# Kernel tuning notes

Measured on AMD Instinct MI355X. Metric: run time of the kernel, lower is better.

## Reference

```python
import jax, jax.numpy as jnp
import numpy as np

# DeformConv (RegSeg): offset conv + mask conv (sigmoid) + modulated deformable conv v2
STRIDE = 1
PAD = 1
DIL = 1
G = 1          # deformable_groups
KH, KW = 3, 3


def _conv(x, w, b):
    # standard NCHW conv, stride/pad/dilation of the module
    y = jax.lax.conv_general_dilated(
        x, w, window_strides=(STRIDE, STRIDE),
        padding=((PAD, PAD), (PAD, PAD)), rhs_dilation=(DIL, DIL),
        dimension_numbers=("NCHW", "OIHW", "NCHW"))
    return y + b[None, :, None, None]


def _deform_conv2d(x, offset, mask, w, b):
    # torchvision DeformConv2d (modulated, v2) semantics
    B, C, H, W = x.shape
    O = w.shape[0]
    K = KH * KW
    Ho = (H + 2 * PAD - DIL * (KH - 1) - 1) // STRIDE + 1
    Wo = (W + 2 * PAD - DIL * (KW - 1) - 1) // STRIDE + 1
    Cg = C // G

    # base sampling grid: p0 + p_k
    ky = jnp.repeat(jnp.arange(KH), KW) * DIL            # [K]
    kx = jnp.tile(jnp.arange(KW), KH) * DIL              # [K]
    oy = jnp.arange(Ho) * STRIDE - PAD                   # [Ho]
    ox = jnp.arange(Wo) * STRIDE - PAD                   # [Wo]
    base_y = (ky[:, None, None] + oy[None, :, None]).astype(x.dtype)  # [K,Ho,1]
    base_x = (kx[:, None, None] + ox[None, None, :]).astype(x.dtype)  # [K,1,Wo]

    off = offset.reshape(B, G, K, 2, Ho, Wo)             # channel layout: g, k, (dy,dx)
    py = base_y[None, None] + off[:, :, :, 0]            # [B,G,K,Ho,Wo]
    px = base_x[None, None] + off[:, :, :, 1]
    m = mask.reshape(B, G, K, Ho, Wo)

    imgf = x.reshape(B * G, Cg, H * W)
    y0 = jnp.floor(py).astype(jnp.int32)
    x0 = jnp.floor(px).astype(jnp.int32)
    ly = py - y0.astype(x.dtype)
    lx = px - x0.astype(x.dtype)

    def corner(iy, ix, wgt):
        # zero-padded bilinear corner: out-of-bounds corners contribute 0
        valid = (iy >= 0) & (iy < H) & (ix >= 0) & (ix < W)
        idx = (jnp.clip(iy, 0, H - 1) * W + jnp.clip(ix, 0, W - 1)).reshape(B * G, -1)
        g = jax.vmap(lambda im, ii: im[:, ii])(imgf, idx)            # [B*G,Cg,K*Ho*Wo]
        g = g.reshape(B, G, Cg, K, Ho, Wo)
        return g * (wgt * valid.astype(x.dtype))[:, :, None]          # [B,G,Cg,K,Ho,Wo]

    val = (corner(y0,     x0,     (1 - ly) * (1 - lx))
         + corner(y0,     x0 + 1, (1 - ly) * lx)
         + corner(y0 + 1, x0,     ly * (1 - lx))
         + corner(y0 + 1, x0 + 1, ly * lx))
    val = val * m[:, :, None]                                         # modulation

    wr = w.reshape(O, G, Cg, K)
    out = jnp.einsum("bgckpq,ogck->bopq", val, wr) + b[None, :, None, None]
    return out


def setup_inputs() -> dict:
    key = jax.random.key(0)
    ks = jax.random.split(key, 8)
    B, C, H, W, O = 4, 128, 96, 96, 128
    K = KH * KW
    fan = 1.0 / np.sqrt(C * K)
    return {
        "x":        jax.random.normal(ks[0], (B, C, H, W), jnp.float32),
        "x2":       jax.random.normal(ks[1], (B, C, H, W), jnp.float32),
        "offset_w": jax.random.normal(ks[2], (2 * G * K, C, KH, KW), jnp.float32) * 0.01,
        "offset_b": jax.random.normal(ks[3], (2 * G * K,), jnp.float32) * 0.01,
        "mask_w":   jax.random.normal(ks[4], (G * K, C, KH, KW), jnp.float32) * 0.05,
        "mask_b":   jnp.zeros((G * K,), jnp.float32),
        "deform_w": jax.random.normal(ks[5], (O, C, KH, KW), jnp.float32) * fan,
        "deform_b": jax.random.normal(ks[6], (O,), jnp.float32) * fan,
    }


def reference(x, x2, offset_w, offset_b, mask_w, mask_b, deform_w, deform_b):
    offset = _conv(x2, offset_w, offset_b)
    mask = jax.nn.sigmoid(_conv(x2, mask_w, mask_b))
    return _deform_conv2d(x, offset, mask, deform_w, deform_b)
```

## Files before the change

kernel.cpp:

```cpp
#include <hip/hip_runtime.h>

#define CIN   128
#define HH    96
#define WW    96
#define OUTC  128
#define HWSZ  9216
#define KK    9
#define KTOT  1152

typedef _Float16 f16x8 __attribute__((ext_vector_type(8)));
typedef _Float16 h2    __attribute__((ext_vector_type(2)));
typedef float    f32x4 __attribute__((ext_vector_type(4)));

__device__ __forceinline__ unsigned short f2h(float f) {
  _Float16 h = (_Float16)f;
  return __builtin_bit_cast(unsigned short, h);
}
__device__ __forceinline__ unsigned pack_h(float v0, float v1) {
  auto r = __builtin_amdgcn_cvt_pkrtz(v0, v1);
  return __builtin_bit_cast(unsigned, r);
}

#define WT2B_O 147456
#define BIAS_O 184320
#define XN_O   184384
#define X2N_O  (184384 + 4718592)

__global__ __launch_bounds__(256) void prep_all(
    const float* __restrict__ x, const float* __restrict__ x2,
    const float* __restrict__ offw, const float* __restrict__ maskw,
    const float* __restrict__ defw, const float* __restrict__ offb,
    const float* __restrict__ maskb, void* __restrict__ wsv) {
  int bid = blockIdx.x;
  int t = threadIdx.x;
  if (bid < 1152) {
    __shared__ unsigned short tile[64][136];
    int tsel = bid / 576;
    int rem = bid - tsel * 576;
    int b = rem / 144;
    int hw0 = (rem % 144) * 64;
    const float* src = tsel ? x2 : x;
    unsigned short* dst = (unsigned short*)wsv + (tsel ? X2N_O : XN_O);
    unsigned* tw = (unsigned*)&tile[0][0];
    int c2  = t & 15;
    int px4 = t >> 4;
#pragma unroll
    for (int pass = 0; pass < 4; ++pass) {
      int c = pass * 32 + c2 * 2;
      const float* r0 = src + ((size_t)(b * CIN + c)) * HWSZ + hw0 + px4 * 4;
      float4 f0 = *(const float4*)r0;
      float4 f1 = *(const float4*)(r0 + HWSZ);
      int wb = pass * 16 + c2;
      tw[(px4 * 4 + 0) * 68 + wb] = pack_h(f0.x, f1.x);
      tw[(px4 * 4 + 1) * 68 + wb] = pack_h(f0.y, f1.y);
      tw[(px4 * 4 + 2) * 68 + wb] = pack_h(f0.z, f1.z);
      tw[(px4 * 4 + 3) * 68 + wb] = pack_h(f0.w, f1.w);
    }
    __syncthreads();
    unsigned* drow = (unsigned*)(dst + ((size_t)(b * HWSZ + hw0)) * 128);
    int w4 = t & 15, pxr = t >> 4;
#pragma unroll
    for (int pass = 0; pass < 4; ++pass) {
      int px = pass * 16 + pxr;
      uint4 v = *(const uint4*)&tw[px * 68 + w4 * 4];
      *(uint4*)&drow[(size_t)px * 64 + w4 * 4] = v;
    }
    return;
  }
  unsigned short* wtb  = (unsigned short*)wsv;
  unsigned short* wt2b = wtb + WT2B_O;
  float* bias32 = (float*)(wtb + BIAS_O);
  int idx = (bid - 1152) * 256 + t;
  if (idx < OUTC * KTOT) {
    int o = idx / KTOT, r = idx - o * KTOT;
    int c = r / KK, tap = r - c * KK;
    wtb[o * KTOT + tap * 128 + c] = f2h(defw[idx]);
  } else if (idx < OUTC * KTOT + 32 * KTOT) {
    int j = idx - OUTC * KTOT;
    int oc = j / KTOT, r = j - oc * KTOT;
    int c = r / KK, tap = r - c * KK;
    float v = 0.f;
    if (oc < 18)      v = offw[j];
    else if (oc < 27) v = maskw[j - 18 * KTOT];
    wt2b[oc * KTOT + tap * 128 + c] = f2h(v);
  } else if (idx < OUTC * KTOT + 32 * KTOT + 32) {
    int j = idx - OUTC * KTOT - 32 * KTOT;
    float v = 0.f;
    if (j < 18) v = offb[j]; else if (j < 27) v = maskb[j - 18];
    bias32[j] = v;
  }
}

__global__ __launch_bounds__(256, 2) void fused(
    const float* __restrict__ defb, const void* __restrict__ wsv,
    float* __restrict__ out) {
  const unsigned short* wtb  = (const unsigned short*)wsv;
  const unsigned short* wt2b = wtb + WT2B_O;
  const float* bias32 = (const float*)(wtb + BIAS_O);
  const unsigned short* xn  = wtb + XN_O;
  const unsigned short* x2n = wtb + X2N_O;

  __shared__ unsigned bwA[64 * 68];
  __shared__ unsigned bwB[64 * 68];
  __shared__ unsigned short val[64][136];
  __shared__ unsigned sidxw[KK * 4 * 64];
  float* om = (float*)&val[0][0];

  int t = threadIdx.x;
  int w = t >> 6;
  int mw = w & 1, nw = w >> 1;
  int l15 = t & 15, quad = (t >> 4) & 3;
  int rb = blockIdx.x;
  int bid = (rb & 7) * 72 + (rb >> 3);
  int b = bid / 144;
  int pblk = (bid % 144) * 64;

  int phg[4], pwg[4];
#pragma unroll
  for (int G = 0; G < 4; ++G) {
    int p = pblk + w * 16 + G * 4 + quad;
    phg[G] = p / WW;
    pwg[G] = p - phg[G] * WW;
  }

  f32x4 oa0 = {0.f, 0.f, 0.f, 0.f};
  f32x4 oa1 = {0.f, 0.f, 0.f, 0.f};
  const unsigned short* x2nb = x2n + ((size_t)b * HWSZ) * 128;
  for (int tap = 0; tap < KK; ++tap) {
    int ky = tap / 3 - 1, kx = tap % 3 - 1;
    uint4 vG[4];
#pragma unroll
    for (int G = 0; G < 4; ++G) {
      int y = phg[G] + ky, xx = pwg[G] + kx;
      bool ok = ((unsigned)y < HH) && ((unsigned)xx < WW);
      int pos = ok ? (y * WW + xx) : 0;
      uint4 v = *(const uint4*)(x2nb + ((size_t)pos << 7) + l15 * 8);
      vG[G] = ok ? v : make_uint4(0u, 0u, 0u, 0u);
    }
#pragma unroll
    for (int j = 0; j < 2; ++j) {
      int cc = t + 256 * j;
      int row = cc >> 4, c16 = cc & 15;
      *(uint4*)&bwA[row * 68 + c16 * 4] =
          *(const uint4*)(wt2b + (size_t)row * KTOT + tap * 128 + c16 * 8);
    }
#pragma unroll
    for (int G = 0; G < 4; ++G)
      *(uint4*)&val[w * 16 + G * 4 + quad][l15 * 8] = vG[G];
    __syncthreads();
#pragma unroll
    for (int ks = 0; ks < 4; ++ks) {
      f16x8 af = *(const f16x8*)&val[w * 16 + l15][ks * 32 + quad * 8];
      f16x8 b0 = *(const f16x8*)&bwA[(size_t)l15 * 68 + ks * 16 + quad * 4];
      f16x8 b1 = *(const f16x8*)&bwA[(size_t)(l15 + 16) * 68 + ks * 16 + quad * 4];
      oa0 = __builtin_amdgcn_mfma_f32_16x16x32_f16(af, b0, oa0, 0, 0, 0);
      oa1 = __builtin_amdgcn_mfma_f32_16x16x32_f16(af, b1, oa1, 0, 0, 0);
    }
    __syncthreads();
  }
#pragma unroll
  for (int nt = 0; nt < 2; ++nt) {
    f32x4 a = nt ? oa1 : oa0;
    int oc = nt * 16 + l15;
    float bia = bias32[oc];
#pragma unroll
    for (int r = 0; r < 4; ++r)
      om[oc * 68 + w * 16 + quad * 4 + r] = a[r] + bia;
  }
  __syncthreads();

  for (int e = t; e < KK * 64; e += 256) {
    int tap = e >> 6, pp = e & 63;
    int gp2 = pblk + pp;
    int h = gp2 / WW, ww_ = gp2 % WW;
    float dy = om[2 * tap * 68 + pp], dx = om[(2 * tap + 1) * 68 + pp];
    float mr = om[(18 + tap) * 68 + pp];
    float m = 1.f / (1.f + __expf(-mr));
    float py  = (float)(h + tap / 3 - 1) + dy;
    float pxx = (float)(ww_ + tap % 3 - 1) + dx;
    float y0f = floorf(py), x0f = floorf(pxx);
    int y0 = (int)y0f, x0 = (int)x0f;
    float ly = py - y0f, lx = pxx - x0f;
    int y1 = y0 + 1, x1 = x0 + 1;
    bool vy0 = (unsigned)y0 < HH, vy1 = (unsigned)y1 < HH;
    bool vx0 = (unsigned)x0 < WW, vx1 = (unsigned)x1 < WW;
    int cy0 = min(max(y0, 0), HH - 1), cy1 = min(max(y1, 0), HH - 1);
    int cx0 = min(max(x0, 0), WW - 1), cx1 = min(max(x1, 0), WW - 1);
    unsigned i00 = cy0 * WW + cx0, i01 = cy0 * WW + cx1;
    unsigned i10 = cy1 * WW + cx0, i11 = cy1 * WW + cx1;
    float w00 = (vy0 && vx0) ? m * (1.f - ly) * (1.f - lx) : 0.f;
    float w01 = (vy0 && vx1) ? m * (1.f - ly) * lx         : 0.f;
    float w10 = (vy1 && vx0) ? m * ly * (1.f - lx)         : 0.f;
    float w11 = (vy1 && vx1) ? m * ly * lx                 : 0.f;
    sidxw[(tap * 4 + 0) * 64 + pp] = i00 | ((unsigned)f2h(w00) << 16);
    sidxw[(tap * 4 + 1) * 64 + pp] = i01 | ((unsigned)f2h(w01) << 16);
    sidxw[(tap * 4 + 2) * 64 + pp] = i10 | ((unsigned)f2h(w10) << 16);
    sidxw[(tap * 4 + 3) * 64 + pp] = i11 | ((unsigned)f2h(w11) << 16);
  }
  __syncthreads();

  f32x4 acc[8];
#pragma unroll
  for (int nt = 0; nt < 8; ++nt) acc[nt] = (f32x4){0.f, 0.f, 0.f, 0.f};
  const unsigned short* xnb = xn + ((size_t)b * HWSZ) * 128;

  auto gatherT = [&](int tap, unsigned sw[4][4], uint4 v[4][4]) {
#pragma unroll
    for (int cr = 0; cr < 4; ++cr)
#pragma unroll
      for (int G = 0; G < 4; ++G)
        sw[cr][G] = sidxw[(tap * 4 + cr) * 64 + w * 16 + G * 4 + quad];
#pragma unroll
    for (int G = 0; G < 4; ++G)
#pragma unroll
      for (int cr = 0; cr < 4; ++cr)
        v[cr][G] = *(const uint4*)(xnb + ((size_t)(sw[cr][G] & 0xffffu) << 7) + l15 * 8);
  };
  auto combineT = [&](unsigned sw[4][4], uint4 v[4][4]) {
#pragma unroll
    for (int G = 0; G < 4; ++G) {
      h2 f[4];
#pragma unroll
      for (int j = 0; j < 4; ++j) f[j] = (h2){(_Float16)0.f, (_Float16)0.f};
#pragma unroll
      for (int cr = 0; cr < 4; ++cr) {
        _Float16 wh =
            __builtin_bit_cast(_Float16, (unsigned short)(sw[cr][G] >> 16));
        h2 wpk = {wh, wh};
        const h2* a = (const h2*)&v[cr][G];
#pragma unroll
        for (int j = 0; j < 4; ++j)
          f[j] += wpk * a[j];
      }
      *(uint4*)&val[w * 16 + G * 4 + quad][l15 * 8] =
          make_uint4(__builtin_bit_cast(unsigned, f[0]),
                     __builtin_bit_cast(unsigned, f[1]),
                     __builtin_bit_cast(unsigned, f[2]),
                     __builtin_bit_cast(unsigned, f[3]));
    }
  };
  auto stageHalf = [&](unsigned* buf, int tap, int half) {
#pragma unroll
    for (int j = 0; j < 4; ++j) {
      int cc = t + 256 * j;
      int row = cc >> 4, c16 = cc & 15;
      *(uint4*)&buf[row * 68 + c16 * 4] =
          *(const uint4*)(wtb + (size_t)(half * 64 + row) * KTOT + tap * 128 + c16 * 8);
    }
  };

  {
    unsigned sw[4][4]; uint4 v[4][4];
    gatherT(0, sw, v);
    combineT(sw, v);
    stageHalf(bwA, 0, 0);
  }
  __syncthreads();

  for (int tap = 0; tap < KK; ++tap) {
    f16x8 af[2][4];
#pragma unroll
    for (int m = 0; m < 2; ++m)
#pragma unroll
      for (int ks = 0; ks < 4; ++ks)
        af[m][ks] =
            *(const f16x8*)&val[mw * 32 + m * 16 + l15][ks * 32 + quad * 8];
    stageHalf(bwB, tap, 1);
#pragma unroll
    for (int m = 0; m < 2; ++m)
#pragma unroll
      for (int ntl = 0; ntl < 2; ++ntl)
#pragma unroll
        for (int ks = 0; ks < 4; ++ks) {
          f16x8 bb = *(const f16x8*)&bwA[(size_t)(nw * 32 + ntl * 16 + l15) * 68 +
                                         ks * 16 + quad * 4];
          acc[m * 2 + ntl] =
              __builtin_amdgcn_mfma_f32_16x16x32_f16(af[m][ks], bb,
                                                     acc[m * 2 + ntl], 0, 0, 0);
        }
    __syncthreads();
    unsigned sw[4][4]; uint4 v[4][4];
    if (tap + 1 < KK) gatherT(tap + 1, sw, v);
#pragma unroll
    for (int m = 0; m < 2; ++m)
#pragma unroll
      for (int ntl = 0; ntl < 2; ++ntl)
#pragma unroll
        for (int ks = 0; ks < 4; ++ks) {
          f16x8 bb = *(const f16x8*)&bwB[(size_t)(nw * 32 + ntl * 16 + l15) * 68 +
                                         ks * 16 + quad * 4];
          acc[4 + m * 2 + ntl] =
              __builtin_amdgcn_mfma_f32_16x16x32_f16(af[m][ks], bb,
                                                     acc[4 + m * 2 + ntl], 0, 0, 0);
        }
    if (tap + 1 < KK) {
      combineT(sw, v);
      stageHalf(bwA, tap + 1, 0);
      __syncthreads();
    }
  }

#pragma unroll
  for (int h = 0; h < 2; ++h)
#pragma unroll
    for (int m = 0; m < 2; ++m)
#pragma unroll
      for (int ntl = 0; ntl < 2; ++ntl) {
        int oc = h * 64 + nw * 32 + ntl * 16 + l15;
        f32x4 a = acc[h * 4 + m * 2 + ntl];
        float db = defb[oc];
        float4 vv = make_float4(a[0] + db, a[1] + db, a[2] + db, a[3] + db);
        *(float4*)&out[((size_t)b * OUTC + oc) * HWSZ + pblk + mw * 32 +
                       m * 16 + quad * 4] = vv;
      }
}

extern "C" void kernel_launch(void* const* d_in, const int* in_sizes, int n_in,
                              void* d_out, int out_size, void* d_ws, size_t ws_size,
                              hipStream_t stream) {
  const float* x     = (const float*)d_in[0];
  const float* x2    = (const float*)d_in[1];
  const float* offw  = (const float*)d_in[2];
  const float* offb  = (const float*)d_in[3];
  const float* maskw = (const float*)d_in[4];
  const float* maskb = (const float*)d_in[5];
  const float* defw  = (const float*)d_in[6];
  const float* defb  = (const float*)d_in[7];
  float* out = (float*)d_out;

  hipLaunchKernelGGL(prep_all, dim3(1873), dim3(256), 0, stream,
                     x, x2, offw, maskw, defw, offb, maskb, d_ws);
  hipLaunchKernelGGL(fused, dim3(576), dim3(256), 0, stream, defb, d_ws, out);
}
```

Before: 153.6 us.

## Split weight staging into quarters and gather in halves to fit three blocks per CU

The output-channel dimension is now staged in four 32-row quarters instead of two 64-row halves. This halves the shared-memory weight buffers and the accumulator and gather register arrays. The bilinear gather for the next tap is split into two halves interleaved between the quarter MFMA passes, and launch bounds are raised to 3 blocks per CU. The aim is more resident blocks (576 blocks fit in one wave at 3 per CU) and better latency hiding, at the cost of extra barriers per tap and re-reading the sampling weights from LDS.

```diff
diff --git a/kernel.cpp b/kernel.cpp
--- a/kernel.cpp
+++ b/kernel.cpp
@@ -91,7 +91,7 @@
   }
 }
 
-__global__ __launch_bounds__(256, 2) void fused(
+__global__ __launch_bounds__(256, 3) void fused(
     const float* __restrict__ defb, const void* __restrict__ wsv,
     float* __restrict__ out) {
   const unsigned short* wtb  = (const unsigned short*)wsv;
@@ -100,8 +100,8 @@
   const unsigned short* xn  = wtb + XN_O;
   const unsigned short* x2n = wtb + X2N_O;
 
-  __shared__ unsigned bwA[64 * 68];
-  __shared__ unsigned bwB[64 * 68];
+  __shared__ unsigned bwA[32 * 68];
+  __shared__ unsigned bwB[32 * 68];
   __shared__ unsigned short val[64][136];
   __shared__ unsigned sidxw[KK * 4 * 64];
   float* om = (float*)&val[0][0];
@@ -199,35 +199,38 @@
   }
   __syncthreads();
 
-  f32x4 acc[8];
-#pragma unroll
-  for (int nt = 0; nt < 8; ++nt) acc[nt] = (f32x4){0.f, 0.f, 0.f, 0.f};
+  f32x4 acc[4][2];
+#pragma unroll
+  for (int q = 0; q < 4; ++q)
+#pragma unroll
+    for (int m = 0; m < 2; ++m) acc[q][m] = (f32x4){0.f, 0.f, 0.f, 0.f};
   const unsigned short* xnb = xn + ((size_t)b * HWSZ) * 128;
 
-  auto gatherT = [&](int tap, unsigned sw[4][4], uint4 v[4][4]) {
-#pragma unroll
-    for (int cr = 0; cr < 4; ++cr)
-#pragma unroll
-      for (int G = 0; G < 4; ++G)
-        sw[cr][G] = sidxw[(tap * 4 + cr) * 64 + w * 16 + G * 4 + quad];
-#pragma unroll
-    for (int G = 0; G < 4; ++G)
-#pragma unroll
-      for (int cr = 0; cr < 4; ++cr)
-        v[cr][G] = *(const uint4*)(xnb + ((size_t)(sw[cr][G] & 0xffffu) << 7) + l15 * 8);
+  auto gatherH = [&](int tap, int h, unsigned sw[2], uint4 v[2][4]) {
+#pragma unroll
+    for (int gi = 0; gi < 2; ++gi) {
+      int G = 2 * h + gi;
+#pragma unroll
+      for (int cr = 0; cr < 4; ++cr) {
+        unsigned s = sidxw[(tap * 4 + cr) * 64 + w * 16 + G * 4 + quad];
+        if (cr == 0) sw[gi] = 0;
+        v[gi][cr] = *(const uint4*)(xnb + ((size_t)(s & 0xffffu) << 7) + l15 * 8);
+      }
+    }
   };
-  auto combineT = [&](unsigned sw[4][4], uint4 v[4][4]) {
-#pragma unroll
-    for (int G = 0; G < 4; ++G) {
+  auto combineH = [&](int tap, int h, uint4 v[2][4]) {
+#pragma unroll
+    for (int gi = 0; gi < 2; ++gi) {
+      int G = 2 * h + gi;
       h2 f[4];
 #pragma unroll
       for (int j = 0; j < 4; ++j) f[j] = (h2){(_Float16)0.f, (_Float16)0.f};
 #pragma unroll
       for (int cr = 0; cr < 4; ++cr) {
-        _Float16 wh =
-            __builtin_bit_cast(_Float16, (unsigned short)(sw[cr][G] >> 16));
+        unsigned s = sidxw[(tap * 4 + cr) * 64 + w * 16 + G * 4 + quad];
+        _Float16 wh = __builtin_bit_cast(_Float16, (unsigned short)(s >> 16));
         h2 wpk = {wh, wh};
-        const h2* a = (const h2*)&v[cr][G];
+        const h2* a = (const h2*)&v[gi][cr];
 #pragma unroll
         for (int j = 0; j < 4; ++j)
           f[j] += wpk * a[j];
@@ -239,25 +242,38 @@
                      __builtin_bit_cast(unsigned, f[3]));
     }
   };
-  auto stageHalf = [&](unsigned* buf, int tap, int half) {
-#pragma unroll
-    for (int j = 0; j < 4; ++j) {
+  auto stageQ = [&](unsigned* buf, int tap, int q) {
+#pragma unroll
+    for (int j = 0; j < 2; ++j) {
       int cc = t + 256 * j;
       int row = cc >> 4, c16 = cc & 15;
       *(uint4*)&buf[row * 68 + c16 * 4] =
-          *(const uint4*)(wtb + (size_t)(half * 64 + row) * KTOT + tap * 128 + c16 * 8);
+          *(const uint4*)(wtb + (size_t)(q * 32 + row) * KTOT + tap * 128 + c16 * 8);
     }
   };
+  auto mfmaQ = [&](const unsigned* buf, f32x4* aq, f16x8 af[2][4]) {
+#pragma unroll
+    for (int ks = 0; ks < 4; ++ks) {
+      f16x8 bb = *(const f16x8*)&buf[(size_t)(nw * 16 + l15) * 68 +
+                                     ks * 16 + quad * 4];
+      aq[0] = __builtin_amdgcn_mfma_f32_16x16x32_f16(af[0][ks], bb, aq[0], 0, 0, 0);
+      aq[1] = __builtin_amdgcn_mfma_f32_16x16x32_f16(af[1][ks], bb, aq[1], 0, 0, 0);
+    }
+  };
 
   {
-    unsigned sw[4][4]; uint4 v[4][4];
-    gatherT(0, sw, v);
-    combineT(sw, v);
-    stageHalf(bwA, 0, 0);
+    unsigned swd[2]; uint4 v0[2][4], v1[2][4];
+    gatherH(0, 0, swd, v0);
+    gatherH(0, 1, swd, v1);
+    combineH(0, 0, v0);
+    combineH(0, 1, v1);
+    stageQ(bwA, 0, 0);
   }
   __syncthreads();
 
   for (int tap = 0; tap < KK; ++tap) {
+    bool more = (tap + 1 < KK);
+    unsigned swd[2]; uint4 v01[2][4], v23[2][4];
     f16x8 af[2][4];
 #pragma unroll
     for (int m = 0; m < 2; ++m)
@@ -265,54 +281,39 @@
       for (int ks = 0; ks < 4; ++ks)
         af[m][ks] =
             *(const f16x8*)&val[mw * 32 + m * 16 + l15][ks * 32 + quad * 8];
-    stageHalf(bwB, tap, 1);
-#pragma unroll
-    for (int m = 0; m < 2; ++m)
-#pragma unroll
-      for (int ntl = 0; ntl < 2; ++ntl)
-#pragma unroll
-        for (int ks = 0; ks < 4; ++ks) {
-          f16x8 bb = *(const f16x8*)&bwA[(size_t)(nw * 32 + ntl * 16 + l15) * 68 +
-                                         ks * 16 + quad * 4];
-          acc[m * 2 + ntl] =
-              __builtin_amdgcn_mfma_f32_16x16x32_f16(af[m][ks], bb,
-                                                     acc[m * 2 + ntl], 0, 0, 0);
-        }
-    __syncthreads();
-    unsigned sw[4][4]; uint4 v[4][4];
-    if (tap + 1 < KK) gatherT(tap + 1, sw, v);
-#pragma unroll
-    for (int m = 0; m < 2; ++m)
-#pragma unroll
-      for (int ntl = 0; ntl < 2; ++ntl)
-#pragma unroll
-        for (int ks = 0; ks < 4; ++ks) {
-          f16x8 bb = *(const f16x8*)&bwB[(size_t)(nw * 32 + ntl * 16 + l15) * 68 +
-                                         ks * 16 + quad * 4];
-          acc[4 + m * 2 + ntl] =
-              __builtin_amdgcn_mfma_f32_16x16x32_f16(af[m][ks], bb,
-                                                     acc[4 + m * 2 + ntl], 0, 0, 0);
-        }
-    if (tap + 1 < KK) {
-      combineT(sw, v);
-      stageHalf(bwA, tap + 1, 0);
-      __syncthreads();
-    }
-  }
-
-#pragma unroll
-  for (int h = 0; h < 2; ++h)
-#pragma unroll
-    for (int m = 0; m < 2; ++m)
-#pragma unroll
-      for (int ntl = 0; ntl < 2; ++ntl) {
-        int oc = h * 64 + nw * 32 + ntl * 16 + l15;
-        f32x4 a = acc[h * 4 + m * 2 + ntl];
-        float db = defb[oc];
-        float4 vv = make_float4(a[0] + db, a[1] + db, a[2] + db, a[3] + db);
-        *(float4*)&out[((size_t)b * OUTC + oc) * HWSZ + pblk + mw * 32 +
-                       m * 16 + quad * 4] = vv;
-      }
+    stageQ(bwB, tap, 1);
+    mfmaQ(bwA, acc[0], af);
+    __syncthreads();
+    if (more) gatherH(tap + 1, 0, swd, v01);
+    stageQ(bwA, tap, 2);
+    mfmaQ(bwB, acc[1], af);
+    __syncthreads();
+    if (more) {
+      combineH(tap + 1, 0, v01);
+      gatherH(tap + 1, 1, swd, v23);
+    }
+    stageQ(bwB, tap, 3);
+    mfmaQ(bwA, acc[2], af);
+    __syncthreads();
+    if (more) {
+      combineH(tap + 1, 1, v23);
+      stageQ(bwA, tap + 1, 0);
+    }
+    mfmaQ(bwB, acc[3], af);
+    if (more) __syncthreads();
+  }
+
+#pragma unroll
+  for (int q = 0; q < 4; ++q)
+#pragma unroll
+    for (int m = 0; m < 2; ++m) {
+      int oc = q * 32 + nw * 16 + l15;
+      f32x4 a = acc[q][m];
+      float db = defb[oc];
+      float4 vv = make_float4(a[0] + db, a[1] + db, a[2] + db, a[3] + db);
+      *(float4*)&out[((size_t)b * OUTC + oc) * HWSZ + pblk + mw * 32 +
+                     m * 16 + quad * 4] = vv;
+    }
 }
 
 extern "C" void kernel_launch(void* const* d_in, const int* in_sizes, int n_in,
```

After: 139.4 us. 9.3% less time.
